# Kernel optimization log

Measured on AMD Instinct MI355X. Metric: run time of the kernel, lower is better.

## Reference

```python
import jax, jax.numpy as jnp
import numpy as np

HIDDEN = 768
HEADS = 12
HEAD_DIM = HIDDEN // HEADS
ORDER = 5


def setup_inputs() -> dict:
    key = jax.random.key(0)
    ks = jax.random.split(key, 8)
    s = 0.02
    return {
        "hidden_states": jax.random.normal(ks[0], (4, 2048, HIDDEN), jnp.float32),
        "Wq": jax.random.normal(ks[1], (HIDDEN, HIDDEN), jnp.float32) * s,
        "bq": jnp.zeros((HIDDEN,), jnp.float32),
        "Wk": jax.random.normal(ks[2], (HIDDEN, HIDDEN), jnp.float32) * s,
        "bk": jnp.zeros((HIDDEN,), jnp.float32),
        "Wv": jax.random.normal(ks[3], (HIDDEN, HIDDEN), jnp.float32) * s,
        "bv": jnp.zeros((HIDDEN,), jnp.float32),
        "alphas": jax.random.normal(ks[4], (HEADS, ORDER + 1), jnp.float32) * s,
    }


def _chebyshev_bias(alphas, seq_len, dtype):
    pos = jnp.arange(seq_len, dtype=dtype)
    # rel[i, j] = j - i, normalized to [-1, 1]
    denom = dtype.type(max(seq_len - 1, 1)) if hasattr(dtype, 'type') else float(max(seq_len - 1, 1))
    x = jnp.clip((pos[None, :] - pos[:, None]) / float(max(seq_len - 1, 1)), -1.0, 1.0)
    t0 = jnp.ones_like(x)
    polys = [t0, x]
    for _ in range(2, ORDER + 1):
        polys.append(2.0 * x * polys[-1] - polys[-2])
    tk = jnp.stack(polys, axis=-1)  # [S, S, order+1]
    return jnp.einsum('hk,ijk->hij', alphas, tk)  # [H, S, S]


def reference(hidden_states, Wq, bq, Wk, bk, Wv, bv, alphas):
    b, s, _ = hidden_states.shape

    def split_heads(t):
        return t.reshape(b, s, HEADS, HEAD_DIM).transpose(0, 2, 1, 3)

    q = split_heads(hidden_states @ Wq.T + bq)  # [B, H, S, D]
    k = split_heads(hidden_states @ Wk.T + bk)
    v = split_heads(hidden_states @ Wv.T + bv)

    scores = jnp.einsum('bhid,bhjd->bhij', q, k) / jnp.sqrt(
        jnp.asarray(HEAD_DIM, hidden_states.dtype))
    scores = scores + _chebyshev_bias(alphas, s, hidden_states.dtype)[None]
    probs = jax.nn.softmax(scores, axis=-1)
    ctx = jnp.einsum('bhij,bhjd->bhid', probs, v)  # [B, H, S, D]
    return ctx.transpose(0, 2, 1, 3).reshape(b, s, HIDDEN)
```

## Files before the change

kernel.cpp:

```cpp
#include <hip/hip_runtime.h>
#include <hip/hip_fp16.h>

#define HIDDEN 768
#define HEADS 12
#define HDIM 64
#define SEQ 2048
#define BATCH 4
#define ORDER 5
#define LOG2E 1.44269504088896f

typedef _Float16 f16;
typedef _Float16 f16x8 __attribute__((ext_vector_type(8)));
typedef _Float16 f16x4 __attribute__((ext_vector_type(4)));
typedef __fp16 fp16x2 __attribute__((ext_vector_type(2)));
typedef float f32x4 __attribute__((ext_vector_type(4)));

#define MFMA16x16x32(A, B, C) __builtin_amdgcn_mfma_f32_16x16x32_f16(A, B, C, 0, 0, 0)

#define GLD16(gptr, lptr)                                                     \
    __builtin_amdgcn_global_load_lds(                                         \
        (const __attribute__((address_space(1))) void*)(gptr),                \
        (__attribute__((address_space(3))) void*)(lptr), 16, 0, 0)

#define NXG (8192 * 768 / 8)
#define NWG (768 * 768 / 8)
#define NCVT (NXG + 3 * NWG)
#define NBIAS (HEADS * (2 * SEQ - 1))

__global__ __launch_bounds__(256)
void prep_kernel(const float* __restrict__ X,
                 const float* __restrict__ Wq, const float* __restrict__ Wk,
                 const float* __restrict__ Wv, const float* __restrict__ alphas,
                 f16* __restrict__ Xh, f16* __restrict__ Wh,
                 float* __restrict__ biasTab)
{
    const int tid = blockIdx.x * 256 + threadIdx.x;
    if (tid < NCVT) {
        const float* src;
        f16* dst;
        size_t off;
        if (tid < NXG)               { src = X;  dst = Xh;              off = (size_t)tid * 8; }
        else if (tid < NXG + NWG)    { src = Wq; dst = Wh;              off = (size_t)(tid - NXG) * 8; }
        else if (tid < NXG + 2*NWG)  { src = Wk; dst = Wh + 768 * 768;  off = (size_t)(tid - NXG - NWG) * 8; }
        else                         { src = Wv; dst = Wh + 2*768*768;  off = (size_t)(tid - NXG - 2*NWG) * 8; }
        float4 a = *(const float4*)(src + off);
        float4 b = *(const float4*)(src + off + 4);
        f16x8 h;
        h[0] = (f16)a.x; h[1] = (f16)a.y; h[2] = (f16)a.z; h[3] = (f16)a.w;
        h[4] = (f16)b.x; h[5] = (f16)b.y; h[6] = (f16)b.z; h[7] = (f16)b.w;
        *(f16x8*)(dst + off) = h;
    } else {
        int idx = tid - NCVT;
        if (idx >= NBIAS) return;
        const int W = 2 * SEQ - 1;
        int h = idx / W;
        int t = idx - h * W;
        float x = (float)(t - (SEQ - 1)) / (float)(SEQ - 1);
        float tp = 1.0f;
        float tc = x;
        float acc = alphas[h * (ORDER + 1) + 0] * tp + alphas[h * (ORDER + 1) + 1] * tc;
#pragma unroll
        for (int k = 2; k <= ORDER; ++k) {
            float tn = 2.0f * x * tc - tp;
            acc += alphas[h * (ORDER + 1) + k] * tn;
            tp = tc; tc = tn;
        }
        biasTab[idx] = acc * LOG2E;
    }
}

__global__ __launch_bounds__(256)
void qkv_kernel(const f16* __restrict__ Xh, const f16* __restrict__ Wh,
                const float* __restrict__ bq, const float* __restrict__ bk,
                const float* __restrict__ bv,
                f16* __restrict__ qf, f16* __restrict__ kf, f16* __restrict__ vtf)
{
    const int wgid = (blockIdx.x & 7) * 144 + (blockIdx.x >> 3);
    const int tileM = wgid / 18;
    const int tileN = wgid % 18;
    const int m0 = tileM * 128;
    const int n0g = tileN * 128;
    const int w = tileN / 6;
    const int nloc0 = n0g - w * 768;
    const float* __restrict__ bias = (w == 0) ? bq : (w == 1) ? bk : bv;

    __shared__ __align__(16) f16 sA[128][32];
    __shared__ __align__(16) f16 sB[128][32];

    const int t = threadIdx.x;
    const int lane = t & 63;
    const int wv = t >> 6;
    const int wm = wv >> 1, wn = wv & 1;
    const int fr = lane & 15;
    const int kg = lane >> 4;

    const int srow = lane >> 2;
    const int scol = (lane & 3) * 8;

    f32x4 acc[4][4];
#pragma unroll
    for (int i = 0; i < 4; ++i)
#pragma unroll
        for (int j = 0; j < 4; ++j) acc[i][j] = (f32x4)(0.0f);

    const f16* gA = Xh + (size_t)(m0 + wv * 32 + srow) * 768 + scol;
    const f16* gB = Wh + (size_t)(n0g + wv * 32 + srow) * 768 + scol;
    f16* lA0 = &sA[wv * 32][0];
    f16* lA1 = &sA[wv * 32 + 16][0];
    f16* lB0 = &sB[wv * 32][0];
    f16* lB1 = &sB[wv * 32 + 16][0];

    for (int kt = 0; kt < 768; kt += 32) {
        __syncthreads();
        GLD16(gA + kt, lA0);
        GLD16(gA + kt + 16 * 768, lA1);
        GLD16(gB + kt, lB0);
        GLD16(gB + kt + 16 * 768, lB1);
        __syncthreads();

        f16x8 af[4], bf[4];
#pragma unroll
        for (int i = 0; i < 4; ++i) {
            af[i] = *(const f16x8*)&sA[wm * 64 + i * 16 + fr][kg * 8];
            bf[i] = *(const f16x8*)&sB[wn * 64 + i * 16 + fr][kg * 8];
        }
#pragma unroll
        for (int mi = 0; mi < 4; ++mi)
#pragma unroll
            for (int ni = 0; ni < 4; ++ni)
                acc[mi][ni] = MFMA16x16x32(af[mi], bf[ni], acc[mi][ni]);
    }

    const int bb = m0 >> 11;
#pragma unroll
    for (int mi = 0; mi < 4; ++mi) {
        const int s0 = (m0 & 2047) + wm * 64 + mi * 16 + kg * 4;
        const int u = s0 & 31;
        const int s0p = (s0 & ~31) | (((u >> 2) & 3) << 3) | (((u >> 4) & 1) << 2);
#pragma unroll
        for (int ni = 0; ni < 4; ++ni) {
            const int nloc = nloc0 + wn * 64 + ni * 16 + fr;
            const int hh = nloc >> 6, d = nloc & 63;
            const size_t bh = (size_t)bb * HEADS + hh;
            const float bc = bias[nloc];
            if (w == 2) {
                f16x4 pv;
#pragma unroll
                for (int r = 0; r < 4; ++r) pv[r] = (f16)(acc[mi][ni][r] + bc);
                *(f16x4*)&vtf[(bh * HDIM + d) * SEQ + s0p] = pv;
            } else if (w == 0) {
#pragma unroll
                for (int r = 0; r < 4; ++r)
                    qf[(bh * SEQ + s0 + r) * HDIM + d] =
                        (f16)((acc[mi][ni][r] + bc) * (0.125f * LOG2E));
            } else {
#pragma unroll
                for (int r = 0; r < 4; ++r)
                    kf[(bh * SEQ + s0 + r) * HDIM + d] = (f16)(acc[mi][ni][r] + bc);
            }
        }
    }
}

struct __align__(16) SMem {
    union {
        struct {
            f16 sK[64][64];
            f16 sVT[64][64];
        } kv;
        float sO[4][16][72];
    } u;
};

__global__ __launch_bounds__(256, 3)
void attn_kernel(const f16* __restrict__ qf, const f16* __restrict__ kf,
                 const f16* __restrict__ vtf, const float* __restrict__ biasTab,
                 float* __restrict__ out)
{
    const int xcd = blockIdx.x & 7;
    const int ii = blockIdx.x >> 3;
    const int qt = ii & 15;
    const int bh = (ii >> 4) * 8 + xcd;
    const int h = bh % HEADS;
    const int b = bh / HEADS;
    const int q0 = qt * 128;

    __shared__ SMem sm;

    const int t = threadIdx.x;
    const int lane = t & 63;
    const int wv = t >> 6;
    const int fr = lane & 15;
    const int kg = lane >> 4;
    const int r7 = fr & 7;

    const int ubl = kg * 4 - wv * 32 - fr + 127;
    const float* const gB = biasTab + (size_t)h * (2 * SEQ - 1) + 1920 - q0 + ubl;

    f16x8 aq[2][2];
#pragma unroll
    for (int s = 0; s < 2; ++s)
#pragma unroll
        for (int c = 0; c < 2; ++c)
            aq[s][c] = *(const f16x8*)(qf +
                ((size_t)bh * SEQ + q0 + wv * 32 + s * 16 + fr) * HDIM + c * 32 + kg * 8);

    f32x4 oacc[2][4];
    float lsum[2] = {0.0f, 0.0f};
#pragma unroll
    for (int s = 0; s < 2; ++s)
#pragma unroll
        for (int df = 0; df < 4; ++df) oacc[s][df] = (f32x4)(0.0f);

    const int srow = t >> 2;
    const int scol = (t & 3) * 16;
    const int sw0 = 8 * (((t & 3) * 2) ^ (srow & 7));
    const int sw1 = 8 * (((t & 3) * 2 + 1) ^ (srow & 7));
    const f16* const gkb = kf + ((size_t)bh * SEQ + srow) * HDIM + scol;
    const f16* const gvb = vtf + ((size_t)bh * HDIM + srow) * SEQ + scol;

    f16x8 rk0, rk1, rv0, rv1;
    auto stage_load = [&](int j0) {
        rk0 = *(const f16x8*)(gkb + (size_t)j0 * HDIM);
        rk1 = *(const f16x8*)(gkb + (size_t)j0 * HDIM + 8);
        rv0 = *(const f16x8*)(gvb + j0);
        rv1 = *(const f16x8*)(gvb + j0 + 8);
    };
    auto stage_write = [&]() {
        *(f16x8*)&sm.u.kv.sK[srow][sw0]  = rk0;
        *(f16x8*)&sm.u.kv.sK[srow][sw1]  = rk1;
        *(f16x8*)&sm.u.kv.sVT[srow][sw0] = rv0;
        *(f16x8*)&sm.u.kv.sVT[srow][sw1] = rv1;
    };

    float rb[5][4];
    auto bias_load = [&](int j0, float (&dst)[5][4]) {
#pragma unroll
        for (int g = 0; g < 5; ++g)
#pragma unroll
            for (int r = 0; r < 4; ++r)
                dst[g][r] = gB[j0 + (g - 1) * 16 + r];
    };

    stage_load(0);
    bias_load(0, rb);
    stage_write();
    __syncthreads();

    for (int j0 = 0; j0 < SEQ; j0 += 64) {
        const bool more = (j0 + 64 < SEQ);
        float rbn[5][4];
        if (more) {
            stage_load(j0 + 64);
            bias_load(j0 + 64, rbn);
        }

        f32x4 tt[2][4];
#pragma unroll
        for (int s = 0; s < 2; ++s)
#pragma unroll
            for (int ni = 0; ni < 4; ++ni)
#pragma unroll
                for (int r = 0; r < 4; ++r) tt[s][ni][r] = rb[ni - s + 1][r];

        __builtin_amdgcn_s_setprio(1);
#pragma unroll
        for (int ni = 0; ni < 4; ++ni) {
            const f16* kb = &sm.u.kv.sK[ni * 16 + fr][0];
            f16x8 bk0 = *(const f16x8*)(kb + 8 * (kg ^ r7));
            f16x8 bk1 = *(const f16x8*)(kb + 8 * ((kg + 4) ^ r7));
            tt[0][ni] = MFMA16x16x32(bk0, aq[0][0], tt[0][ni]);
            tt[0][ni] = MFMA16x16x32(bk1, aq[0][1], tt[0][ni]);
            tt[1][ni] = MFMA16x16x32(bk0, aq[1][0], tt[1][ni]);
            tt[1][ni] = MFMA16x16x32(bk1, aq[1][1], tt[1][ni]);
        }
        __builtin_amdgcn_s_setprio(0);

        union { fp16x2 h2[4]; f16x8 v8; } ap[2][2];
#pragma unroll
        for (int s = 0; s < 2; ++s) {
            float ls = 0.0f;
            float pv[4][4];
#pragma unroll
            for (int ni = 0; ni < 4; ++ni)
#pragma unroll
                for (int r = 0; r < 4; ++r) {
                    float p = __builtin_amdgcn_exp2f(tt[s][ni][r]);
                    pv[ni][r] = p;
                    ls += p;
                }
#pragma unroll
            for (int m = 0; m < 2; ++m)
#pragma unroll
                for (int nr = 0; nr < 2; ++nr) {
                    const int ni = 2 * m + nr;
                    ap[s][m].h2[nr * 2 + 0] =
                        __builtin_amdgcn_cvt_pkrtz(pv[ni][0], pv[ni][1]);
                    ap[s][m].h2[nr * 2 + 1] =
                        __builtin_amdgcn_cvt_pkrtz(pv[ni][2], pv[ni][3]);
                }
            lsum[s] += ls;
        }

        __builtin_amdgcn_s_setprio(1);
#pragma unroll
        for (int df = 0; df < 4; ++df) {
            const f16* vb = &sm.u.kv.sVT[df * 16 + fr][0];
            f16x8 bv0 = *(const f16x8*)(vb + 8 * (kg ^ r7));
            f16x8 bv1 = *(const f16x8*)(vb + 8 * ((kg + 4) ^ r7));
            oacc[0][df] = MFMA16x16x32(bv0, ap[0][0].v8, oacc[0][df]);
            oacc[0][df] = MFMA16x16x32(bv1, ap[0][1].v8, oacc[0][df]);
            oacc[1][df] = MFMA16x16x32(bv0, ap[1][0].v8, oacc[1][df]);
            oacc[1][df] = MFMA16x16x32(bv1, ap[1][1].v8, oacc[1][df]);
        }
        __builtin_amdgcn_s_setprio(0);

        __syncthreads();
        if (more) {
            stage_write();
#pragma unroll
            for (int g = 0; g < 5; ++g)
#pragma unroll
                for (int r = 0; r < 4; ++r) rb[g][r] = rbn[g][r];
            __syncthreads();
        }
    }

    float inv[2];
#pragma unroll
    for (int s = 0; s < 2; ++s) {
        float l = lsum[s];
        l += __shfl_xor(l, 16, 64);
        l += __shfl_xor(l, 32, 64);
        inv[s] = 1.0f / l;
    }

    __syncthreads();
#pragma unroll
    for (int s = 0; s < 2; ++s) {
#pragma unroll
        for (int df = 0; df < 4; ++df) {
            f32x4 v = oacc[s][df];
            v *= inv[s];
            *(f32x4*)&sm.u.sO[wv][fr][df * 16 + kg * 4] = v;
        }
        int row = lane >> 2;
        int cb = (lane & 3) * 16;
        float* dst = out + ((size_t)b * SEQ + q0 + wv * 32 + s * 16 + row) * HIDDEN
                         + h * HDIM + cb;
#pragma unroll
        for (int i = 0; i < 4; ++i) {
            f32x4 v = *(const f32x4*)&sm.u.sO[wv][row][cb + 4 * i];
            *(f32x4*)(dst + 4 * i) = v;
        }
    }
}

extern "C" void kernel_launch(void* const* d_in, const int* in_sizes, int n_in,
                              void* d_out, int out_size, void* d_ws, size_t ws_size,
                              hipStream_t stream) {
    const float* X      = (const float*)d_in[0];
    const float* Wq     = (const float*)d_in[1];
    const float* bq     = (const float*)d_in[2];
    const float* Wk     = (const float*)d_in[3];
    const float* bk     = (const float*)d_in[4];
    const float* Wv     = (const float*)d_in[5];
    const float* bv     = (const float*)d_in[6];
    const float* alphas = (const float*)d_in[7];
    float* out = (float*)d_out;

    const size_t nQ = (size_t)BATCH * HEADS * SEQ * HDIM;
    f16* qf  = (f16*)d_ws;
    f16* kf  = qf + nQ;
    f16* vtf = kf + nQ;
    float* biasTab = (float*)(vtf + nQ);
    f16* Xh = (f16*)(biasTab + 49152);
    f16* Wh = Xh + (size_t)8192 * 768;

    const int prep_threads = NCVT + NBIAS;
    hipLaunchKernelGGL(prep_kernel, dim3((prep_threads + 255) / 256), dim3(256), 0,
                       stream, X, Wq, Wk, Wv, alphas, Xh, Wh, biasTab);
    hipLaunchKernelGGL(qkv_kernel, dim3(1152), dim3(256), 0, stream,
                       Xh, Wh, bq, bk, bv, qf, kf, vtf);
    hipLaunchKernelGGL(attn_kernel, dim3(BATCH * HEADS * 16), dim3(256), 0, stream,
                       qf, kf, vtf, biasTab, out);
}
```

Before: 127.2 us.

## Double-buffer K/V tiles in LDS to halve barriers per tile

Splits the shared K/V staging into two buffers (A/B) and unrolls the key loop by two tiles. The next tile is written to the alternate buffer right after the QK MFMAs rather than after a barrier, so each tile needs one barrier instead of two. This doubles the LDS used for K/V from 16 KB to 32 KB, which could lower occupancy at launch_bounds(256,3).

```diff
diff --git a/kernel.cpp b/kernel.cpp
--- a/kernel.cpp
+++ b/kernel.cpp
@@ -165,8 +165,10 @@
 struct __align__(16) SMem {
     union {
         struct {
-            f16 sK[64][64];
-            f16 sVT[64][64];
+            f16 KA[64][64];
+            f16 VA[64][64];
+            f16 KB[64][64];
+            f16 VB[64][64];
         } kv;
         float sO[4][16][72];
     } u;
@@ -226,11 +228,11 @@
         rv0 = *(const f16x8*)(gvb + j0);
         rv1 = *(const f16x8*)(gvb + j0 + 8);
     };
-    auto stage_write = [&]() {
-        *(f16x8*)&sm.u.kv.sK[srow][sw0]  = rk0;
-        *(f16x8*)&sm.u.kv.sK[srow][sw1]  = rk1;
-        *(f16x8*)&sm.u.kv.sVT[srow][sw0] = rv0;
-        *(f16x8*)&sm.u.kv.sVT[srow][sw1] = rv1;
+    auto stage_write = [&](f16 (&K)[64][64], f16 (&V)[64][64]) {
+        *(f16x8*)&K[srow][sw0] = rk0;
+        *(f16x8*)&K[srow][sw1] = rk1;
+        *(f16x8*)&V[srow][sw0] = rv0;
+        *(f16x8*)&V[srow][sw1] = rv1;
     };
 
     float rb[5][4];
@@ -242,19 +244,8 @@
                 dst[g][r] = gB[j0 + (g - 1) * 16 + r];
     };
 
-    stage_load(0);
-    bias_load(0, rb);
-    stage_write();
-    __syncthreads();
-
-    for (int j0 = 0; j0 < SEQ; j0 += 64) {
-        const bool more = (j0 + 64 < SEQ);
-        float rbn[5][4];
-        if (more) {
-            stage_load(j0 + 64);
-            bias_load(j0 + 64, rbn);
-        }
-
+    auto process = [&](const f16 (&K)[64][64], const f16 (&V)[64][64],
+                       f16 (&Kn)[64][64], f16 (&Vn)[64][64], bool wr) {
         f32x4 tt[2][4];
 #pragma unroll
         for (int s = 0; s < 2; ++s)
@@ -266,7 +257,7 @@
         __builtin_amdgcn_s_setprio(1);
 #pragma unroll
         for (int ni = 0; ni < 4; ++ni) {
-            const f16* kb = &sm.u.kv.sK[ni * 16 + fr][0];
+            const f16* kb = &K[ni * 16 + fr][0];
             f16x8 bk0 = *(const f16x8*)(kb + 8 * (kg ^ r7));
             f16x8 bk1 = *(const f16x8*)(kb + 8 * ((kg + 4) ^ r7));
             tt[0][ni] = MFMA16x16x32(bk0, aq[0][0], tt[0][ni]);
@@ -275,6 +266,8 @@
             tt[1][ni] = MFMA16x16x32(bk1, aq[1][1], tt[1][ni]);
         }
         __builtin_amdgcn_s_setprio(0);
+
+        if (wr) stage_write(Kn, Vn);
 
         union { fp16x2 h2[4]; f16x8 v8; } ap[2][2];
 #pragma unroll
@@ -305,7 +298,7 @@
         __builtin_amdgcn_s_setprio(1);
 #pragma unroll
         for (int df = 0; df < 4; ++df) {
-            const f16* vb = &sm.u.kv.sVT[df * 16 + fr][0];
+            const f16* vb = &V[df * 16 + fr][0];
             f16x8 bv0 = *(const f16x8*)(vb + 8 * (kg ^ r7));
             f16x8 bv1 = *(const f16x8*)(vb + 8 * ((kg + 4) ^ r7));
             oacc[0][df] = MFMA16x16x32(bv0, ap[0][0].v8, oacc[0][df]);
@@ -314,16 +307,37 @@
             oacc[1][df] = MFMA16x16x32(bv1, ap[1][1].v8, oacc[1][df]);
         }
         __builtin_amdgcn_s_setprio(0);
-
+    };
+
+    stage_load(0);
+    bias_load(0, rb);
+    stage_write(sm.u.kv.KA, sm.u.kv.VA);
+    __syncthreads();
+
+    float rbn[5][4];
+    for (int jj = 0; jj < SEQ; jj += 128) {
+        stage_load(jj + 64);
+        bias_load(jj + 64, rbn);
+        process(sm.u.kv.KA, sm.u.kv.VA, sm.u.kv.KB, sm.u.kv.VB, true);
+#pragma unroll
+        for (int g = 0; g < 5; ++g)
+#pragma unroll
+            for (int r = 0; r < 4; ++r) rb[g][r] = rbn[g][r];
         __syncthreads();
+
+        const bool more = (jj + 128 < SEQ);
         if (more) {
-            stage_write();
+            stage_load(jj + 128);
+            bias_load(jj + 128, rbn);
+        }
+        process(sm.u.kv.KB, sm.u.kv.VB, sm.u.kv.KA, sm.u.kv.VA, more);
+        if (more) {
 #pragma unroll
             for (int g = 0; g < 5; ++g)
 #pragma unroll
                 for (int r = 0; r < 4; ++r) rb[g][r] = rbn[g][r];
-            __syncthreads();
-        }
+        }
+        __syncthreads();
     }
 
     float inv[2];
@@ -335,7 +349,6 @@
         inv[s] = 1.0f / l;
     }
 
-    __syncthreads();
 #pragma unroll
     for (int s = 0; s < 2; ++s) {
 #pragma unroll
```

Result: slower. 183.1 us (+43.9%).
